# Performance work log

Measured on AMD Instinct MI355X. Metric: run time of the kernel, lower is better.

The kernel has to match this reference:

```python
import jax, jax.numpy as jnp
import numpy as np

BS, N, D_IN, D_OUT = 4, 512, 64, 64
TEMP = 1.0
POOL_K = 0.5
N_KEEP = max(int(N * POOL_K), 1)  # 256
BN_EPS = 1e-5


def setup_inputs() -> dict:
    key = jax.random.key(0)
    ks = jax.random.split(key, 12)
    xav = lambda k, shape: jax.random.normal(k, shape, jnp.float32) * np.sqrt(2.0 / sum(shape))
    return {
        "x": jax.random.normal(ks[0], (BS, N, D_IN), jnp.float32),
        "att_proj_w": xav(ks[1], (D_IN, D_OUT)),
        "att_proj_b": jnp.zeros((D_OUT,), jnp.float32),
        "att_weight": xav(ks[2], (D_OUT, 1))[:, 0],  # (D_OUT,)
        "pwa_w": xav(ks[3], (D_IN, D_OUT)),
        "pwa_b": jnp.zeros((D_OUT,), jnp.float32),
        "pwoa_w": xav(ks[4], (D_IN, D_OUT)),
        "pwoa_b": jnp.zeros((D_OUT,), jnp.float32),
        "bn_gamma": jnp.ones((D_OUT,), jnp.float32),
        "bn_beta": jnp.zeros((D_OUT,), jnp.float32),
        "bn_mean": jnp.zeros((D_OUT,), jnp.float32),
        "bn_var": jnp.ones((D_OUT,), jnp.float32),
        "pool_w": xav(ks[5], (D_OUT, 1))[:, 0],  # (D_OUT,)
        "pool_b": jnp.zeros((), jnp.float32),
    }


def reference(x, att_proj_w, att_proj_b, att_weight, pwa_w, pwa_b,
              pwoa_w, pwoa_b, bn_gamma, bn_beta, bn_mean, bn_var,
              pool_w, pool_b):
    # ---- GraphAttentionLayer (eval mode: dropout off, BN uses running stats) ----
    # pairwise node product: (bs, i, j, d)
    pair = x[:, :, None, :] * x[:, None, :, :]
    a = jnp.tanh(jnp.einsum('bijd,de->bije', pair, att_proj_w) + att_proj_b)
    scores = jnp.einsum('bije,e->bij', a, att_weight) / TEMP
    att = jax.nn.softmax(scores, axis=-1)  # torch softmax over dim=-2 of (bs,i,j,1) == j axis
    agg = jnp.einsum('bij,bjd->bid', att, x)
    h = (agg @ pwa_w + pwa_b) + (x @ pwoa_w + pwoa_b)
    h = (h - bn_mean) * jax.lax.rsqrt(bn_var + BN_EPS) * bn_gamma + bn_beta
    h = jax.nn.selu(h)
    # ---- GraphPool (eval: dropout off) ----
    s = jax.nn.sigmoid(h @ pool_w + pool_b)  # (bs, N)
    _, idx = jax.lax.top_k(s, N_KEEP)        # (bs, N_KEEP), sorted desc like torch.topk
    hs = h * s[..., None]
    out = jnp.take_along_axis(hs, idx[..., None], axis=1)  # (bs, N_KEEP, D_OUT)
    return out
```

## Files before the change

### kernel.cpp

```cpp
#include <hip/hip_runtime.h>
#include <hip/hip_bf16.h>
#include <math.h>

#define BSZ 4
#define NN 512
#define DD 64
#define NKEEP 256

typedef __attribute__((ext_vector_type(8))) short short8;
typedef __attribute__((ext_vector_type(4))) float f32x4;

__device__ __forceinline__ ushort f2bf_rne(float f) {
  union { float f; unsigned u; } v; v.f = f;
  unsigned r = v.u + 0x7fffu + ((v.u >> 16) & 1u);
  return (ushort)(r >> 16);
}
__device__ __forceinline__ float bf2f(ushort h) {
  union { unsigned u; float f; } v; v.u = ((unsigned)h) << 16;
  return v.f;
}
__device__ __forceinline__ void split2t(float a, float b, uint& hu, uint& lu) {
  const uint au = __float_as_uint(a), bu = __float_as_uint(b);
  hu = (au >> 16) | (bu & 0xffff0000u);
  const float ra = a - __uint_as_float(au & 0xffff0000u);
  const float rb = b - __uint_as_float(bu & 0xffff0000u);
  lu = (__float_as_uint(ra) >> 16) | (__float_as_uint(rb) & 0xffff0000u);
}

__global__ __launch_bounds__(256) void k_score(
    const float* __restrict__ x, const float* __restrict__ apw,
    const float* __restrict__ apb, const float* __restrict__ aw,
    float* __restrict__ sT) {
  __shared__ __align__(16) float T[4][8][16];

  const int w = threadIdx.x >> 6;
  const int l = threadIdx.x & 63;
  const int il = l & 15, g = l >> 4;

  short8 wfh[4][2], wfl[4][2];
  #pragma unroll
  for (int eq = 0; eq < 4; ++eq)
    #pragma unroll
    for (int ks = 0; ks < 2; ++ks) {
      short8 hh, ll;
      #pragma unroll
      for (int q = 0; q < 8; ++q) {
        const int d = ks * 32 + g * 8 + q;
        const float wv = apw[d * 64 + eq * 16 + il];
        const ushort h = f2bf_rne(wv);
        hh[q] = (short)h;
        ll[q] = (short)f2bf_rne(wv - bf2f(h));
      }
      wfh[eq][ks] = hh; wfl[eq][ks] = ll;
    }

  const float K2 = 2.8853900817779268f;
  float aw2_4[4], bK2[4], awq = 0.f;
  #pragma unroll
  for (int eq = 0; eq < 4; ++eq) {
    const float a = aw[eq * 16 + il];
    aw2_4[eq] = 2.f * a;
    bK2[eq] = apb[eq * 16 + il] * K2;
    awq += a;
  }
  awq += __shfl_xor(awq, 1, 64);
  awq += __shfl_xor(awq, 2, 64);
  awq += __shfl_xor(awq, 4, 64);
  awq += __shfl_xor(awq, 8, 64);
  const float awC = awq;

  const int wave_id = blockIdx.x * 4 + w;

  for (int task = wave_id; task < 4224; task += 2048) {
    const int b = task / 1056;
    const int pid = task - b * 1056;
    int it = 0, rem = pid;
    while (rem >= 32 - (it >> 1)) { rem -= 32 - (it >> 1); ++it; }
    const int jt = (it >> 1) + rem;
    const int i0 = it * 8, j0 = jt * 16;
    const bool diag = ((it >> 1) == jt);

    const float* xb = x + (size_t)b * NN * DD;
    float* plane = sT + (size_t)b * NN * NN;

    const float* xjr = xb + (size_t)(j0 + il) * DD;
    const float4 xj0 = *reinterpret_cast<const float4*>(xjr + g * 8);
    const float4 xj1 = *reinterpret_cast<const float4*>(xjr + g * 8 + 4);
    const float4 xj2 = *reinterpret_cast<const float4*>(xjr + 32 + g * 8);
    const float4 xj3 = *reinterpret_cast<const float4*>(xjr + 32 + g * 8 + 4);

    #pragma unroll 2
    for (int ii = 0; ii < 8; ++ii) {
      const int i_glob = i0 + ii;
      const float* xir = xb + (size_t)i_glob * DD;
      const float4 xi0 = *reinterpret_cast<const float4*>(xir + g * 8);
      const float4 xi1 = *reinterpret_cast<const float4*>(xir + g * 8 + 4);
      const float4 xi2 = *reinterpret_cast<const float4*>(xir + 32 + g * 8);
      const float4 xi3 = *reinterpret_cast<const float4*>(xir + 32 + g * 8 + 4);

      union { uint u[4]; short8 s; } hA, lA, hB, lB;
      split2t(xj0.x * xi0.x, xj0.y * xi0.y, hA.u[0], lA.u[0]);
      split2t(xj0.z * xi0.z, xj0.w * xi0.w, hA.u[1], lA.u[1]);
      split2t(xj1.x * xi1.x, xj1.y * xi1.y, hA.u[2], lA.u[2]);
      split2t(xj1.z * xi1.z, xj1.w * xi1.w, hA.u[3], lA.u[3]);
      split2t(xj2.x * xi2.x, xj2.y * xi2.y, hB.u[0], lB.u[0]);
      split2t(xj2.z * xi2.z, xj2.w * xi2.w, hB.u[1], lB.u[1]);
      split2t(xj3.x * xi3.x, xj3.y * xi3.y, hB.u[2], lB.u[2]);
      split2t(xj3.z * xi3.z, xj3.w * xi3.w, hB.u[3], lB.u[3]);

      f32x4 acc[4];
      #pragma unroll
      for (int eq = 0; eq < 4; ++eq) acc[eq] = (f32x4){0.f, 0.f, 0.f, 0.f};
      #pragma unroll
      for (int eq = 0; eq < 4; ++eq) {
        acc[eq] = __builtin_amdgcn_mfma_f32_16x16x32_bf16(hA.s, wfh[eq][0], acc[eq], 0, 0, 0);
        acc[eq] = __builtin_amdgcn_mfma_f32_16x16x32_bf16(hA.s, wfl[eq][0], acc[eq], 0, 0, 0);
        acc[eq] = __builtin_amdgcn_mfma_f32_16x16x32_bf16(lA.s, wfh[eq][0], acc[eq], 0, 0, 0);
        acc[eq] = __builtin_amdgcn_mfma_f32_16x16x32_bf16(hB.s, wfh[eq][1], acc[eq], 0, 0, 0);
        acc[eq] = __builtin_amdgcn_mfma_f32_16x16x32_bf16(hB.s, wfl[eq][1], acc[eq], 0, 0, 0);
        acc[eq] = __builtin_amdgcn_mfma_f32_16x16x32_bf16(lB.s, wfh[eq][1], acc[eq], 0, 0, 0);
      }

      float neg[4] = {0.f, 0.f, 0.f, 0.f};
      #pragma unroll
      for (int eq = 0; eq < 4; ++eq)
        #pragma unroll
        for (int rr = 0; rr < 4; ++rr) {
          const float ex = __builtin_amdgcn_exp2f(fmaf(acc[eq][rr], K2, bK2[eq]));
          const float rc = __builtin_amdgcn_rcpf(ex + 1.0f);
          neg[rr] = fmaf(aw2_4[eq], rc, neg[rr]);
        }
      #pragma unroll
      for (int rr = 0; rr < 4; ++rr) {
        neg[rr] += __shfl_xor(neg[rr], 1, 64);
        neg[rr] += __shfl_xor(neg[rr], 2, 64);
        neg[rr] += __shfl_xor(neg[rr], 4, 64);
        neg[rr] += __shfl_xor(neg[rr], 8, 64);
      }
      const f32x4 sc = {awC - neg[0], awC - neg[1], awC - neg[2], awC - neg[3]};

      if (il == 0) {
        if (!diag) {
          *reinterpret_cast<f32x4*>(plane + (size_t)i_glob * NN + j0 + g * 4) = sc;
        } else {
          #pragma unroll
          for (int rr = 0; rr < 4; ++rr) {
            const int jv = j0 + g * 4 + rr;
            if (jv >= i_glob) plane[(size_t)i_glob * NN + jv] = sc[rr];
          }
        }
        *reinterpret_cast<f32x4*>(&T[w][ii][g * 4]) = sc;
      }
    }

    {
      const int jv = l >> 2;
      const int ip = (l & 3) * 2;
      const float m0 = T[w][ip + 0][jv];
      const float m1 = T[w][ip + 1][jv];
      const int jr = j0 + jv;
      if (!diag) {
        const float2 mv = {m0, m1};
        *reinterpret_cast<float2*>(plane + (size_t)jr * NN + i0 + ip) = mv;
      } else {
        if (jr > i0 + ip + 0) plane[(size_t)jr * NN + i0 + ip + 0] = m0;
        if (jr > i0 + ip + 1) plane[(size_t)jr * NN + i0 + ip + 1] = m1;
      }
    }
  }
}

__global__ __launch_bounds__(256) void k_soft(
    const float* __restrict__ x, const float* __restrict__ sT,
    const float* __restrict__ pwa, const float* __restrict__ pwab,
    const float* __restrict__ pwoa, const float* __restrict__ pwob,
    const float* __restrict__ gam, const float* __restrict__ bet,
    const float* __restrict__ mu, const float* __restrict__ var,
    const float* __restrict__ poolw, const float* __restrict__ poolb,
    float* __restrict__ h, float* __restrict__ s) {
  __shared__ float ssc[2][512];
  __shared__ float srm[2][4], srs[2][4];
  __shared__ float sagg[4][2][64];
  __shared__ float rag[2][64], xis[2][64];

  const int t = threadIdx.x;
  const int w = t >> 6, l = t & 63;
  const int jw = w * 128;

  for (int task = blockIdx.x; task < 1024; task += 512) {
    const int b = task >> 8;
    const int rp = task & 255;
    const int i_r0 = rp * 2, i_r1 = i_r0 + 1;
    const float* xb = x + (size_t)b * NN * DD;
    const float* pl0 = sT + (size_t)b * NN * NN;

    const size_t o0 = (size_t)i_r0 * NN + jw + l;
    const size_t o1 = (size_t)i_r1 * NN + jw + l;
    float r0a = pl0[o0];
    float r0b = pl0[o0 + 64];
    float r1a = pl0[o1];
    float r1b = pl0[o1 + 64];
    float m0 = fmaxf(r0a, r0b), m1 = fmaxf(r1a, r1b);
    #pragma unroll
    for (int off = 32; off; off >>= 1) {
      m0 = fmaxf(m0, __shfl_xor(m0, off, 64));
      m1 = fmaxf(m1, __shfl_xor(m1, off, 64));
    }
    if (l == 0) { srm[0][w] = m0; srm[1][w] = m1; }
    __syncthreads();
    m0 = fmaxf(fmaxf(srm[0][0], srm[0][1]), fmaxf(srm[0][2], srm[0][3]));
    m1 = fmaxf(fmaxf(srm[1][0], srm[1][1]), fmaxf(srm[1][2], srm[1][3]));

    const float L2E = 1.4426950408889634f;
    float e0a = __builtin_amdgcn_exp2f((r0a - m0) * L2E);
    float e0b = __builtin_amdgcn_exp2f((r0b - m0) * L2E);
    float e1a = __builtin_amdgcn_exp2f((r1a - m1) * L2E);
    float e1b = __builtin_amdgcn_exp2f((r1b - m1) * L2E);
    float ps0 = e0a + e0b, ps1 = e1a + e1b;
    #pragma unroll
    for (int off = 32; off; off >>= 1) {
      ps0 += __shfl_xor(ps0, off, 64);
      ps1 += __shfl_xor(ps1, off, 64);
    }
    if (l == 0) { srs[0][w] = ps0; srs[1][w] = ps1; }
    __syncthreads();
    const float inv0 = 1.f / (srs[0][0] + srs[0][1] + srs[0][2] + srs[0][3]);
    const float inv1 = 1.f / (srs[1][0] + srs[1][1] + srs[1][2] + srs[1][3]);
    ssc[0][jw + l] = e0a * inv0;
    ssc[0][jw + 64 + l] = e0b * inv0;
    ssc[1][jw + l] = e1a * inv1;
    ssc[1][jw + 64 + l] = e1b * inv1;
    __syncthreads();

    float g0a = 0.f, g0b = 0.f, g1a = 0.f, g1b = 0.f;
    #pragma unroll 4
    for (int jj = 0; jj < 128; jj += 2) {
      const int j = jw + jj;
      const float xv0 = xb[(size_t)j * DD + l];
      const float xv1 = xb[(size_t)(j + 1) * DD + l];
      g0a = fmaf(ssc[0][j], xv0, g0a);
      g1a = fmaf(ssc[1][j], xv0, g1a);
      g0b = fmaf(ssc[0][j + 1], xv1, g0b);
      g1b = fmaf(ssc[1][j + 1], xv1, g1b);
    }
    sagg[w][0][l] = g0a + g0b;
    sagg[w][1][l] = g1a + g1b;
    __syncthreads();

    if (w < 2) {
      const int irow = i_r0 + w;
      rag[w][l] = sagg[0][w][l] + sagg[1][w][l] + sagg[2][w][l] + sagg[3][w][l];
      xis[w][l] = xb[(size_t)irow * DD + l];
      float acc = 0.f;
      #pragma unroll 8
      for (int d = 0; d < 64; ++d) {
        acc = fmaf(rag[w][d], pwa[d * 64 + l], acc);
        acc = fmaf(xis[w][d], pwoa[d * 64 + l], acc);
      }
      acc += pwab[l] + pwob[l];
      float hb = (acc - mu[l]) * rsqrtf(var[l] + 1e-5f) * gam[l] + bet[l];
      const float SC = 1.0507009873554805f, AL = 1.6732632423543772f;
      float hv = hb > 0.f ? SC * hb : SC * AL * expm1f(hb);
      h[((size_t)(b * NN + irow)) * DD + l] = hv;

      float p = hv * poolw[l];
      #pragma unroll
      for (int off = 32; off; off >>= 1) p += __shfl_xor(p, off, 64);
      if (l == 0) s[b * NN + irow] = 1.f / (1.f + expf(-(p + poolb[0])));
    }
    __syncthreads();
  }
}

__global__ __launch_bounds__(512) void k_sel(
    const float* __restrict__ s, const float* __restrict__ h,
    float* __restrict__ out) {
  __shared__ float svv[NN];
  __shared__ int inv[NKEEP];
  __shared__ float sval[NKEEP];
  const int b = blockIdx.x, t = threadIdx.x;
  svv[t] = s[b * NN + t];
  __syncthreads();

  const float my = svv[t];
  int r = 0;
  #pragma unroll 4
  for (int j0 = 0; j0 < NN; j0 += 4) {
    float4 v = *reinterpret_cast<const float4*>(&svv[j0]);
    r += (v.x > my) || (v.x == my && (j0 + 0) < t);
    r += (v.y > my) || (v.y == my && (j0 + 1) < t);
    r += (v.z > my) || (v.z == my && (j0 + 2) < t);
    r += (v.w > my) || (v.w == my && (j0 + 3) < t);
  }
  if (r < NKEEP) { inv[r] = t; sval[r] = my; }
  __syncthreads();

  #pragma unroll
  for (int pos = t; pos < NKEEP * 16; pos += 512) {
    const int kk = pos >> 4, d4 = (pos & 15) * 4;
    const int i = inv[kk];
    const float sc = sval[kk];
    float4 v = *reinterpret_cast<const float4*>(
        h + ((size_t)(b * NN + i)) * DD + d4);
    v.x *= sc; v.y *= sc; v.z *= sc; v.w *= sc;
    *reinterpret_cast<float4*>(out + ((size_t)(b * NKEEP + kk)) * DD + d4) = v;
  }
}

extern "C" void kernel_launch(void* const* d_in, const int* in_sizes, int n_in,
                              void* d_out, int out_size, void* d_ws, size_t ws_size,
                              hipStream_t stream) {
  const float* x     = (const float*)d_in[0];
  const float* apw   = (const float*)d_in[1];
  const float* apb   = (const float*)d_in[2];
  const float* aw    = (const float*)d_in[3];
  const float* pwa   = (const float*)d_in[4];
  const float* pwab  = (const float*)d_in[5];
  const float* pwoa  = (const float*)d_in[6];
  const float* pwob  = (const float*)d_in[7];
  const float* gam   = (const float*)d_in[8];
  const float* bet   = (const float*)d_in[9];
  const float* mu    = (const float*)d_in[10];
  const float* var   = (const float*)d_in[11];
  const float* poolw = (const float*)d_in[12];
  const float* poolb = (const float*)d_in[13];
  float* out = (float*)d_out;

  float* sT = (float*)d_ws;
  float* h  = sT + (size_t)BSZ * NN * NN;
  float* s  = h + (size_t)BSZ * NN * DD;

  k_score<<<512, 256, 0, stream>>>(x, apw, apb, aw, sT);
  k_soft<<<512, 256, 0, stream>>>(x, sT, pwa, pwab, pwoa, pwob,
                                  gam, bet, mu, var, poolw, poolb, h, s);
  k_sel<<<BSZ, 512, 0, stream>>>(s, h, out);
}
```

Before: 67.02 us.

## Fuse three kernels into one persistent kernel with atomic grid barriers

Merges the score, softmax/aggregation, and top-k selection kernels into a single 512-block launch. Stages are separated by a software grid barrier built on an atomic counter, which is reset by a memset before each launch. This removes two kernel-launch gaps and inter-kernel drain, but adds the cost of spin barriers and a memset. It also relies on all 512 blocks being co-resident, otherwise the barrier deadlocks. The selection stage now runs on 256 threads, each handling two elements.

```diff
diff --git a/kernel.cpp b/kernel.cpp
--- a/kernel.cpp
+++ b/kernel.cpp
@@ -6,6 +6,7 @@
 #define NN 512
 #define DD 64
 #define NKEEP 256
+#define NBLK 512
 
 typedef __attribute__((ext_vector_type(8))) short short8;
 typedef __attribute__((ext_vector_type(4))) float f32x4;
@@ -27,283 +28,297 @@
   lu = (__float_as_uint(ra) >> 16) | (__float_as_uint(rb) & 0xffff0000u);
 }
 
-__global__ __launch_bounds__(256) void k_score(
+__device__ __forceinline__ void grid_barrier(int* cnt, int phase) {
+  __syncthreads();
+  if (threadIdx.x == 0) {
+    __threadfence();
+    atomicAdd(&cnt[phase], 1);
+    while (atomicAdd(&cnt[phase], 0) < NBLK) __builtin_amdgcn_s_sleep(1);
+    __threadfence();
+  }
+  __syncthreads();
+}
+
+__global__ __launch_bounds__(256) void k_fused(
     const float* __restrict__ x, const float* __restrict__ apw,
     const float* __restrict__ apb, const float* __restrict__ aw,
-    float* __restrict__ sT) {
-  __shared__ __align__(16) float T[4][8][16];
-
-  const int w = threadIdx.x >> 6;
-  const int l = threadIdx.x & 63;
-  const int il = l & 15, g = l >> 4;
-
-  short8 wfh[4][2], wfl[4][2];
-  #pragma unroll
-  for (int eq = 0; eq < 4; ++eq)
-    #pragma unroll
-    for (int ks = 0; ks < 2; ++ks) {
-      short8 hh, ll;
-      #pragma unroll
-      for (int q = 0; q < 8; ++q) {
-        const int d = ks * 32 + g * 8 + q;
-        const float wv = apw[d * 64 + eq * 16 + il];
-        const ushort h = f2bf_rne(wv);
-        hh[q] = (short)h;
-        ll[q] = (short)f2bf_rne(wv - bf2f(h));
-      }
-      wfh[eq][ks] = hh; wfl[eq][ks] = ll;
-    }
-
-  const float K2 = 2.8853900817779268f;
-  float aw2_4[4], bK2[4], awq = 0.f;
-  #pragma unroll
-  for (int eq = 0; eq < 4; ++eq) {
-    const float a = aw[eq * 16 + il];
-    aw2_4[eq] = 2.f * a;
-    bK2[eq] = apb[eq * 16 + il] * K2;
-    awq += a;
-  }
-  awq += __shfl_xor(awq, 1, 64);
-  awq += __shfl_xor(awq, 2, 64);
-  awq += __shfl_xor(awq, 4, 64);
-  awq += __shfl_xor(awq, 8, 64);
-  const float awC = awq;
-
-  const int wave_id = blockIdx.x * 4 + w;
-
-  for (int task = wave_id; task < 4224; task += 2048) {
-    const int b = task / 1056;
-    const int pid = task - b * 1056;
-    int it = 0, rem = pid;
-    while (rem >= 32 - (it >> 1)) { rem -= 32 - (it >> 1); ++it; }
-    const int jt = (it >> 1) + rem;
-    const int i0 = it * 8, j0 = jt * 16;
-    const bool diag = ((it >> 1) == jt);
-
-    const float* xb = x + (size_t)b * NN * DD;
-    float* plane = sT + (size_t)b * NN * NN;
-
-    const float* xjr = xb + (size_t)(j0 + il) * DD;
-    const float4 xj0 = *reinterpret_cast<const float4*>(xjr + g * 8);
-    const float4 xj1 = *reinterpret_cast<const float4*>(xjr + g * 8 + 4);
-    const float4 xj2 = *reinterpret_cast<const float4*>(xjr + 32 + g * 8);
-    const float4 xj3 = *reinterpret_cast<const float4*>(xjr + 32 + g * 8 + 4);
-
-    #pragma unroll 2
-    for (int ii = 0; ii < 8; ++ii) {
-      const int i_glob = i0 + ii;
-      const float* xir = xb + (size_t)i_glob * DD;
-      const float4 xi0 = *reinterpret_cast<const float4*>(xir + g * 8);
-      const float4 xi1 = *reinterpret_cast<const float4*>(xir + g * 8 + 4);
-      const float4 xi2 = *reinterpret_cast<const float4*>(xir + 32 + g * 8);
-      const float4 xi3 = *reinterpret_cast<const float4*>(xir + 32 + g * 8 + 4);
-
-      union { uint u[4]; short8 s; } hA, lA, hB, lB;
-      split2t(xj0.x * xi0.x, xj0.y * xi0.y, hA.u[0], lA.u[0]);
-      split2t(xj0.z * xi0.z, xj0.w * xi0.w, hA.u[1], lA.u[1]);
-      split2t(xj1.x * xi1.x, xj1.y * xi1.y, hA.u[2], lA.u[2]);
-      split2t(xj1.z * xi1.z, xj1.w * xi1.w, hA.u[3], lA.u[3]);
-      split2t(xj2.x * xi2.x, xj2.y * xi2.y, hB.u[0], lB.u[0]);
-      split2t(xj2.z * xi2.z, xj2.w * xi2.w, hB.u[1], lB.u[1]);
-      split2t(xj3.x * xi3.x, xj3.y * xi3.y, hB.u[2], lB.u[2]);
-      split2t(xj3.z * xi3.z, xj3.w * xi3.w, hB.u[3], lB.u[3]);
-
-      f32x4 acc[4];
-      #pragma unroll
-      for (int eq = 0; eq < 4; ++eq) acc[eq] = (f32x4){0.f, 0.f, 0.f, 0.f};
-      #pragma unroll
-      for (int eq = 0; eq < 4; ++eq) {
-        acc[eq] = __builtin_amdgcn_mfma_f32_16x16x32_bf16(hA.s, wfh[eq][0], acc[eq], 0, 0, 0);
-        acc[eq] = __builtin_amdgcn_mfma_f32_16x16x32_bf16(hA.s, wfl[eq][0], acc[eq], 0, 0, 0);
-        acc[eq] = __builtin_amdgcn_mfma_f32_16x16x32_bf16(lA.s, wfh[eq][0], acc[eq], 0, 0, 0);
-        acc[eq] = __builtin_amdgcn_mfma_f32_16x16x32_bf16(hB.s, wfh[eq][1], acc[eq], 0, 0, 0);
-        acc[eq] = __builtin_amdgcn_mfma_f32_16x16x32_bf16(hB.s, wfl[eq][1], acc[eq], 0, 0, 0);
-        acc[eq] = __builtin_amdgcn_mfma_f32_16x16x32_bf16(lB.s, wfh[eq][1], acc[eq], 0, 0, 0);
-      }
-
-      float neg[4] = {0.f, 0.f, 0.f, 0.f};
-      #pragma unroll
-      for (int eq = 0; eq < 4; ++eq)
-        #pragma unroll
-        for (int rr = 0; rr < 4; ++rr) {
-          const float ex = __builtin_amdgcn_exp2f(fmaf(acc[eq][rr], K2, bK2[eq]));
-          const float rc = __builtin_amdgcn_rcpf(ex + 1.0f);
-          neg[rr] = fmaf(aw2_4[eq], rc, neg[rr]);
-        }
-      #pragma unroll
-      for (int rr = 0; rr < 4; ++rr) {
-        neg[rr] += __shfl_xor(neg[rr], 1, 64);
-        neg[rr] += __shfl_xor(neg[rr], 2, 64);
-        neg[rr] += __shfl_xor(neg[rr], 4, 64);
-        neg[rr] += __shfl_xor(neg[rr], 8, 64);
-      }
-      const f32x4 sc = {awC - neg[0], awC - neg[1], awC - neg[2], awC - neg[3]};
-
-      if (il == 0) {
-        if (!diag) {
-          *reinterpret_cast<f32x4*>(plane + (size_t)i_glob * NN + j0 + g * 4) = sc;
-        } else {
-          #pragma unroll
-          for (int rr = 0; rr < 4; ++rr) {
-            const int jv = j0 + g * 4 + rr;
-            if (jv >= i_glob) plane[(size_t)i_glob * NN + jv] = sc[rr];
-          }
-        }
-        *reinterpret_cast<f32x4*>(&T[w][ii][g * 4]) = sc;
-      }
-    }
-
-    {
-      const int jv = l >> 2;
-      const int ip = (l & 3) * 2;
-      const float m0 = T[w][ip + 0][jv];
-      const float m1 = T[w][ip + 1][jv];
-      const int jr = j0 + jv;
-      if (!diag) {
-        const float2 mv = {m0, m1};
-        *reinterpret_cast<float2*>(plane + (size_t)jr * NN + i0 + ip) = mv;
-      } else {
-        if (jr > i0 + ip + 0) plane[(size_t)jr * NN + i0 + ip + 0] = m0;
-        if (jr > i0 + ip + 1) plane[(size_t)jr * NN + i0 + ip + 1] = m1;
-      }
-    }
-  }
-}
-
-__global__ __launch_bounds__(256) void k_soft(
-    const float* __restrict__ x, const float* __restrict__ sT,
     const float* __restrict__ pwa, const float* __restrict__ pwab,
     const float* __restrict__ pwoa, const float* __restrict__ pwob,
     const float* __restrict__ gam, const float* __restrict__ bet,
     const float* __restrict__ mu, const float* __restrict__ var,
     const float* __restrict__ poolw, const float* __restrict__ poolb,
-    float* __restrict__ h, float* __restrict__ s) {
+    float* __restrict__ sT, float* __restrict__ h, float* __restrict__ s,
+    int* __restrict__ cnt, float* __restrict__ out) {
+  __shared__ __align__(16) float T[4][8][16];
   __shared__ float ssc[2][512];
   __shared__ float srm[2][4], srs[2][4];
   __shared__ float sagg[4][2][64];
   __shared__ float rag[2][64], xis[2][64];
-
-  const int t = threadIdx.x;
-  const int w = t >> 6, l = t & 63;
-  const int jw = w * 128;
-
-  for (int task = blockIdx.x; task < 1024; task += 512) {
-    const int b = task >> 8;
-    const int rp = task & 255;
-    const int i_r0 = rp * 2, i_r1 = i_r0 + 1;
-    const float* xb = x + (size_t)b * NN * DD;
-    const float* pl0 = sT + (size_t)b * NN * NN;
-
-    const size_t o0 = (size_t)i_r0 * NN + jw + l;
-    const size_t o1 = (size_t)i_r1 * NN + jw + l;
-    float r0a = pl0[o0];
-    float r0b = pl0[o0 + 64];
-    float r1a = pl0[o1];
-    float r1b = pl0[o1 + 64];
-    float m0 = fmaxf(r0a, r0b), m1 = fmaxf(r1a, r1b);
-    #pragma unroll
-    for (int off = 32; off; off >>= 1) {
-      m0 = fmaxf(m0, __shfl_xor(m0, off, 64));
-      m1 = fmaxf(m1, __shfl_xor(m1, off, 64));
-    }
-    if (l == 0) { srm[0][w] = m0; srm[1][w] = m1; }
-    __syncthreads();
-    m0 = fmaxf(fmaxf(srm[0][0], srm[0][1]), fmaxf(srm[0][2], srm[0][3]));
-    m1 = fmaxf(fmaxf(srm[1][0], srm[1][1]), fmaxf(srm[1][2], srm[1][3]));
-
-    const float L2E = 1.4426950408889634f;
-    float e0a = __builtin_amdgcn_exp2f((r0a - m0) * L2E);
-    float e0b = __builtin_amdgcn_exp2f((r0b - m0) * L2E);
-    float e1a = __builtin_amdgcn_exp2f((r1a - m1) * L2E);
-    float e1b = __builtin_amdgcn_exp2f((r1b - m1) * L2E);
-    float ps0 = e0a + e0b, ps1 = e1a + e1b;
-    #pragma unroll
-    for (int off = 32; off; off >>= 1) {
-      ps0 += __shfl_xor(ps0, off, 64);
-      ps1 += __shfl_xor(ps1, off, 64);
-    }
-    if (l == 0) { srs[0][w] = ps0; srs[1][w] = ps1; }
-    __syncthreads();
-    const float inv0 = 1.f / (srs[0][0] + srs[0][1] + srs[0][2] + srs[0][3]);
-    const float inv1 = 1.f / (srs[1][0] + srs[1][1] + srs[1][2] + srs[1][3]);
-    ssc[0][jw + l] = e0a * inv0;
-    ssc[0][jw + 64 + l] = e0b * inv0;
-    ssc[1][jw + l] = e1a * inv1;
-    ssc[1][jw + 64 + l] = e1b * inv1;
-    __syncthreads();
-
-    float g0a = 0.f, g0b = 0.f, g1a = 0.f, g1b = 0.f;
-    #pragma unroll 4
-    for (int jj = 0; jj < 128; jj += 2) {
-      const int j = jw + jj;
-      const float xv0 = xb[(size_t)j * DD + l];
-      const float xv1 = xb[(size_t)(j + 1) * DD + l];
-      g0a = fmaf(ssc[0][j], xv0, g0a);
-      g1a = fmaf(ssc[1][j], xv0, g1a);
-      g0b = fmaf(ssc[0][j + 1], xv1, g0b);
-      g1b = fmaf(ssc[1][j + 1], xv1, g1b);
-    }
-    sagg[w][0][l] = g0a + g0b;
-    sagg[w][1][l] = g1a + g1b;
-    __syncthreads();
-
-    if (w < 2) {
-      const int irow = i_r0 + w;
-      rag[w][l] = sagg[0][w][l] + sagg[1][w][l] + sagg[2][w][l] + sagg[3][w][l];
-      xis[w][l] = xb[(size_t)irow * DD + l];
-      float acc = 0.f;
-      #pragma unroll 8
-      for (int d = 0; d < 64; ++d) {
-        acc = fmaf(rag[w][d], pwa[d * 64 + l], acc);
-        acc = fmaf(xis[w][d], pwoa[d * 64 + l], acc);
-      }
-      acc += pwab[l] + pwob[l];
-      float hb = (acc - mu[l]) * rsqrtf(var[l] + 1e-5f) * gam[l] + bet[l];
-      const float SC = 1.0507009873554805f, AL = 1.6732632423543772f;
-      float hv = hb > 0.f ? SC * hb : SC * AL * expm1f(hb);
-      h[((size_t)(b * NN + irow)) * DD + l] = hv;
-
-      float p = hv * poolw[l];
-      #pragma unroll
-      for (int off = 32; off; off >>= 1) p += __shfl_xor(p, off, 64);
-      if (l == 0) s[b * NN + irow] = 1.f / (1.f + expf(-(p + poolb[0])));
-    }
-    __syncthreads();
-  }
-}
-
-__global__ __launch_bounds__(512) void k_sel(
-    const float* __restrict__ s, const float* __restrict__ h,
-    float* __restrict__ out) {
   __shared__ float svv[NN];
   __shared__ int inv[NKEEP];
   __shared__ float sval[NKEEP];
-  const int b = blockIdx.x, t = threadIdx.x;
-  svv[t] = s[b * NN + t];
-  __syncthreads();
-
-  const float my = svv[t];
-  int r = 0;
-  #pragma unroll 4
-  for (int j0 = 0; j0 < NN; j0 += 4) {
-    float4 v = *reinterpret_cast<const float4*>(&svv[j0]);
-    r += (v.x > my) || (v.x == my && (j0 + 0) < t);
-    r += (v.y > my) || (v.y == my && (j0 + 1) < t);
-    r += (v.z > my) || (v.z == my && (j0 + 2) < t);
-    r += (v.w > my) || (v.w == my && (j0 + 3) < t);
+
+  const int t = threadIdx.x;
+  const int w = t >> 6, l = t & 63;
+  const int il = l & 15, g = l >> 4;
+
+  {
+    short8 wfh[4][2], wfl[4][2];
+    #pragma unroll
+    for (int eq = 0; eq < 4; ++eq)
+      #pragma unroll
+      for (int ks = 0; ks < 2; ++ks) {
+        short8 hh, ll;
+        #pragma unroll
+        for (int q = 0; q < 8; ++q) {
+          const int d = ks * 32 + g * 8 + q;
+          const float wv = apw[d * 64 + eq * 16 + il];
+          const ushort hv = f2bf_rne(wv);
+          hh[q] = (short)hv;
+          ll[q] = (short)f2bf_rne(wv - bf2f(hv));
+        }
+        wfh[eq][ks] = hh; wfl[eq][ks] = ll;
+      }
+
+    const float K2 = 2.8853900817779268f;
+    float aw2_4[4], bK2[4], awq = 0.f;
+    #pragma unroll
+    for (int eq = 0; eq < 4; ++eq) {
+      const float a = aw[eq * 16 + il];
+      aw2_4[eq] = 2.f * a;
+      bK2[eq] = apb[eq * 16 + il] * K2;
+      awq += a;
+    }
+    awq += __shfl_xor(awq, 1, 64);
+    awq += __shfl_xor(awq, 2, 64);
+    awq += __shfl_xor(awq, 4, 64);
+    awq += __shfl_xor(awq, 8, 64);
+    const float awC = awq;
+
+    const int wave_id = blockIdx.x * 4 + w;
+    for (int task = wave_id; task < 4224; task += 2048) {
+      const int b = task / 1056;
+      const int pid = task - b * 1056;
+      int it = 0, rem = pid;
+      while (rem >= 32 - (it >> 1)) { rem -= 32 - (it >> 1); ++it; }
+      const int jt = (it >> 1) + rem;
+      const int i0 = it * 8, j0 = jt * 16;
+      const bool diag = ((it >> 1) == jt);
+
+      const float* xb = x + (size_t)b * NN * DD;
+      float* plane = sT + (size_t)b * NN * NN;
+
+      const float* xjr = xb + (size_t)(j0 + il) * DD;
+      const float4 xj0 = *reinterpret_cast<const float4*>(xjr + g * 8);
+      const float4 xj1 = *reinterpret_cast<const float4*>(xjr + g * 8 + 4);
+      const float4 xj2 = *reinterpret_cast<const float4*>(xjr + 32 + g * 8);
+      const float4 xj3 = *reinterpret_cast<const float4*>(xjr + 32 + g * 8 + 4);
+
+      #pragma unroll 2
+      for (int ii = 0; ii < 8; ++ii) {
+        const int i_glob = i0 + ii;
+        const float* xir = xb + (size_t)i_glob * DD;
+        const float4 xi0 = *reinterpret_cast<const float4*>(xir + g * 8);
+        const float4 xi1 = *reinterpret_cast<const float4*>(xir + g * 8 + 4);
+        const float4 xi2 = *reinterpret_cast<const float4*>(xir + 32 + g * 8);
+        const float4 xi3 = *reinterpret_cast<const float4*>(xir + 32 + g * 8 + 4);
+
+        union { uint u[4]; short8 s; } hA, lA, hB, lB;
+        split2t(xj0.x * xi0.x, xj0.y * xi0.y, hA.u[0], lA.u[0]);
+        split2t(xj0.z * xi0.z, xj0.w * xi0.w, hA.u[1], lA.u[1]);
+        split2t(xj1.x * xi1.x, xj1.y * xi1.y, hA.u[2], lA.u[2]);
+        split2t(xj1.z * xi1.z, xj1.w * xi1.w, hA.u[3], lA.u[3]);
+        split2t(xj2.x * xi2.x, xj2.y * xi2.y, hB.u[0], lB.u[0]);
+        split2t(xj2.z * xi2.z, xj2.w * xi2.w, hB.u[1], lB.u[1]);
+        split2t(xj3.x * xi3.x, xj3.y * xi3.y, hB.u[2], lB.u[2]);
+        split2t(xj3.z * xi3.z, xj3.w * xi3.w, hB.u[3], lB.u[3]);
+
+        f32x4 acc[4];
+        #pragma unroll
+        for (int eq = 0; eq < 4; ++eq) acc[eq] = (f32x4){0.f, 0.f, 0.f, 0.f};
+        #pragma unroll
+        for (int eq = 0; eq < 4; ++eq) {
+          acc[eq] = __builtin_amdgcn_mfma_f32_16x16x32_bf16(hA.s, wfh[eq][0], acc[eq], 0, 0, 0);
+          acc[eq] = __builtin_amdgcn_mfma_f32_16x16x32_bf16(hA.s, wfl[eq][0], acc[eq], 0, 0, 0);
+          acc[eq] = __builtin_amdgcn_mfma_f32_16x16x32_bf16(lA.s, wfh[eq][0], acc[eq], 0, 0, 0);
+          acc[eq] = __builtin_amdgcn_mfma_f32_16x16x32_bf16(hB.s, wfh[eq][1], acc[eq], 0, 0, 0);
+          acc[eq] = __builtin_amdgcn_mfma_f32_16x16x32_bf16(hB.s, wfl[eq][1], acc[eq], 0, 0, 0);
+          acc[eq] = __builtin_amdgcn_mfma_f32_16x16x32_bf16(lB.s, wfh[eq][1], acc[eq], 0, 0, 0);
+        }
+
+        float neg[4] = {0.f, 0.f, 0.f, 0.f};
+        #pragma unroll
+        for (int eq = 0; eq < 4; ++eq)
+          #pragma unroll
+          for (int rr = 0; rr < 4; ++rr) {
+            const float ex = __builtin_amdgcn_exp2f(fmaf(acc[eq][rr], K2, bK2[eq]));
+            const float rc = __builtin_amdgcn_rcpf(ex + 1.0f);
+            neg[rr] = fmaf(aw2_4[eq], rc, neg[rr]);
+          }
+        #pragma unroll
+        for (int rr = 0; rr < 4; ++rr) {
+          neg[rr] += __shfl_xor(neg[rr], 1, 64);
+          neg[rr] += __shfl_xor(neg[rr], 2, 64);
+          neg[rr] += __shfl_xor(neg[rr], 4, 64);
+          neg[rr] += __shfl_xor(neg[rr], 8, 64);
+        }
+        const f32x4 sc = {awC - neg[0], awC - neg[1], awC - neg[2], awC - neg[3]};
+
+        if (il == 0) {
+          if (!diag) {
+            *reinterpret_cast<f32x4*>(plane + (size_t)i_glob * NN + j0 + g * 4) = sc;
+          } else {
+            #pragma unroll
+            for (int rr = 0; rr < 4; ++rr) {
+              const int jv = j0 + g * 4 + rr;
+              if (jv >= i_glob) plane[(size_t)i_glob * NN + jv] = sc[rr];
+            }
+          }
+          *reinterpret_cast<f32x4*>(&T[w][ii][g * 4]) = sc;
+        }
+      }
+
+      {
+        const int jv = l >> 2;
+        const int ip = (l & 3) * 2;
+        const float m0 = T[w][ip + 0][jv];
+        const float m1 = T[w][ip + 1][jv];
+        const int jr = j0 + jv;
+        if (!diag) {
+          const float2 mv = {m0, m1};
+          *reinterpret_cast<float2*>(plane + (size_t)jr * NN + i0 + ip) = mv;
+        } else {
+          if (jr > i0 + ip + 0) plane[(size_t)jr * NN + i0 + ip + 0] = m0;
+          if (jr > i0 + ip + 1) plane[(size_t)jr * NN + i0 + ip + 1] = m1;
+        }
+      }
+    }
   }
-  if (r < NKEEP) { inv[r] = t; sval[r] = my; }
-  __syncthreads();
-
-  #pragma unroll
-  for (int pos = t; pos < NKEEP * 16; pos += 512) {
-    const int kk = pos >> 4, d4 = (pos & 15) * 4;
-    const int i = inv[kk];
-    const float sc = sval[kk];
-    float4 v = *reinterpret_cast<const float4*>(
-        h + ((size_t)(b * NN + i)) * DD + d4);
-    v.x *= sc; v.y *= sc; v.z *= sc; v.w *= sc;
-    *reinterpret_cast<float4*>(out + ((size_t)(b * NKEEP + kk)) * DD + d4) = v;
+
+  grid_barrier(cnt, 0);
+
+  {
+    const int jw = w * 128;
+    for (int task = blockIdx.x; task < 1024; task += NBLK) {
+      const int b = task >> 8;
+      const int rp = task & 255;
+      const int i_r0 = rp * 2, i_r1 = i_r0 + 1;
+      const float* xb = x + (size_t)b * NN * DD;
+      const float* pl0 = sT + (size_t)b * NN * NN;
+
+      const size_t o0 = (size_t)i_r0 * NN + jw + l;
+      const size_t o1 = (size_t)i_r1 * NN + jw + l;
+      float r0a = pl0[o0];
+      float r0b = pl0[o0 + 64];
+      float r1a = pl0[o1];
+      float r1b = pl0[o1 + 64];
+      float m0 = fmaxf(r0a, r0b), m1 = fmaxf(r1a, r1b);
+      #pragma unroll
+      for (int off = 32; off; off >>= 1) {
+        m0 = fmaxf(m0, __shfl_xor(m0, off, 64));
+        m1 = fmaxf(m1, __shfl_xor(m1, off, 64));
+      }
+      if (l == 0) { srm[0][w] = m0; srm[1][w] = m1; }
+      __syncthreads();
+      m0 = fmaxf(fmaxf(srm[0][0], srm[0][1]), fmaxf(srm[0][2], srm[0][3]));
+      m1 = fmaxf(fmaxf(srm[1][0], srm[1][1]), fmaxf(srm[1][2], srm[1][3]));
+
+      const float L2E = 1.4426950408889634f;
+      float e0a = __builtin_amdgcn_exp2f((r0a - m0) * L2E);
+      float e0b = __builtin_amdgcn_exp2f((r0b - m0) * L2E);
+      float e1a = __builtin_amdgcn_exp2f((r1a - m1) * L2E);
+      float e1b = __builtin_amdgcn_exp2f((r1b - m1) * L2E);
+      float ps0 = e0a + e0b, ps1 = e1a + e1b;
+      #pragma unroll
+      for (int off = 32; off; off >>= 1) {
+        ps0 += __shfl_xor(ps0, off, 64);
+        ps1 += __shfl_xor(ps1, off, 64);
+      }
+      if (l == 0) { srs[0][w] = ps0; srs[1][w] = ps1; }
+      __syncthreads();
+      const float inv0 = 1.f / (srs[0][0] + srs[0][1] + srs[0][2] + srs[0][3]);
+      const float inv1 = 1.f / (srs[1][0] + srs[1][1] + srs[1][2] + srs[1][3]);
+      ssc[0][jw + l] = e0a * inv0;
+      ssc[0][jw + 64 + l] = e0b * inv0;
+      ssc[1][jw + l] = e1a * inv1;
+      ssc[1][jw + 64 + l] = e1b * inv1;
+      __syncthreads();
+
+      float g0a = 0.f, g0b = 0.f, g1a = 0.f, g1b = 0.f;
+      #pragma unroll 4
+      for (int jj = 0; jj < 128; jj += 2) {
+        const int j = jw + jj;
+        const float xv0 = xb[(size_t)j * DD + l];
+        const float xv1 = xb[(size_t)(j + 1) * DD + l];
+        g0a = fmaf(ssc[0][j], xv0, g0a);
+        g1a = fmaf(ssc[1][j], xv0, g1a);
+        g0b = fmaf(ssc[0][j + 1], xv1, g0b);
+        g1b = fmaf(ssc[1][j + 1], xv1, g1b);
+      }
+      sagg[w][0][l] = g0a + g0b;
+      sagg[w][1][l] = g1a + g1b;
+      __syncthreads();
+
+      if (w < 2) {
+        const int irow = i_r0 + w;
+        rag[w][l] = sagg[0][w][l] + sagg[1][w][l] + sagg[2][w][l] + sagg[3][w][l];
+        xis[w][l] = xb[(size_t)irow * DD + l];
+        float acc = 0.f;
+        #pragma unroll 8
+        for (int d = 0; d < 64; ++d) {
+          acc = fmaf(rag[w][d], pwa[d * 64 + l], acc);
+          acc = fmaf(xis[w][d], pwoa[d * 64 + l], acc);
+        }
+        acc += pwab[l] + pwob[l];
+        float hb = (acc - mu[l]) * rsqrtf(var[l] + 1e-5f) * gam[l] + bet[l];
+        const float SC = 1.0507009873554805f, AL = 1.6732632423543772f;
+        float hv = hb > 0.f ? SC * hb : SC * AL * expm1f(hb);
+        h[((size_t)(b * NN + irow)) * DD + l] = hv;
+
+        float p = hv * poolw[l];
+        #pragma unroll
+        for (int off = 32; off; off >>= 1) p += __shfl_xor(p, off, 64);
+        if (l == 0) s[b * NN + irow] = 1.f / (1.f + expf(-(p + poolb[0])));
+      }
+      __syncthreads();
+    }
+  }
+
+  grid_barrier(cnt, 1);
+
+  if (blockIdx.x < BSZ) {
+    const int b = blockIdx.x;
+    svv[t] = s[b * NN + t];
+    svv[t + 256] = s[b * NN + t + 256];
+    __syncthreads();
+
+    const float my0 = svv[t], my1 = svv[t + 256];
+    int r0 = 0, r1 = 0;
+    #pragma unroll 4
+    for (int j0 = 0; j0 < NN; j0 += 4) {
+      float4 v = *reinterpret_cast<const float4*>(&svv[j0]);
+      r0 += (v.x > my0) || (v.x == my0 && (j0 + 0) < t);
+      r0 += (v.y > my0) || (v.y == my0 && (j0 + 1) < t);
+      r0 += (v.z > my0) || (v.z == my0 && (j0 + 2) < t);
+      r0 += (v.w > my0) || (v.w == my0 && (j0 + 3) < t);
+      r1 += (v.x > my1) || (v.x == my1 && (j0 + 0) < t + 256);
+      r1 += (v.y > my1) || (v.y == my1 && (j0 + 1) < t + 256);
+      r1 += (v.z > my1) || (v.z == my1 && (j0 + 2) < t + 256);
+      r1 += (v.w > my1) || (v.w == my1 && (j0 + 3) < t + 256);
+    }
+    if (r0 < NKEEP) { inv[r0] = t; sval[r0] = my0; }
+    if (r1 < NKEEP) { inv[r1] = t + 256; sval[r1] = my1; }
+    __syncthreads();
+
+    for (int pos = t; pos < NKEEP * 16; pos += 256) {
+      const int kk = pos >> 4, d4 = (pos & 15) * 4;
+      const int i = inv[kk];
+      const float sc = sval[kk];
+      float4 v = *reinterpret_cast<const float4*>(
+          h + ((size_t)(b * NN + i)) * DD + d4);
+      v.x *= sc; v.y *= sc; v.z *= sc; v.w *= sc;
+      *reinterpret_cast<float4*>(out + ((size_t)(b * NKEEP + kk)) * DD + d4) = v;
+    }
   }
 }
 
@@ -329,9 +344,10 @@
   float* sT = (float*)d_ws;
   float* h  = sT + (size_t)BSZ * NN * NN;
   float* s  = h + (size_t)BSZ * NN * DD;
-
-  k_score<<<512, 256, 0, stream>>>(x, apw, apb, aw, sT);
-  k_soft<<<512, 256, 0, stream>>>(x, sT, pwa, pwab, pwoa, pwob,
-                                  gam, bet, mu, var, poolw, poolb, h, s);
-  k_sel<<<BSZ, 512, 0, stream>>>(s, h, out);
-}
+  int* cnt  = (int*)(s + BSZ * NN);
+
+  hipMemsetAsync(cnt, 0, 8 * sizeof(int), stream);
+  k_fused<<<NBLK, 256, 0, stream>>>(x, apw, apb, aw, pwa, pwab, pwoa, pwob,
+                                    gam, bet, mu, var, poolw, poolb,
+                                    sT, h, s, cnt, out);
+}
```

After: 178.3 us. 166% more time.
